# Kernel optimization log

Measured on AMD Instinct MI355X. Metric: run time of the kernel, lower is better.

## Reference

```python
import jax, jax.numpy as jnp
import numpy as np

V, C, H, L, E, D, B, T = 32000, 1024, 16, 3, 8, 1024, 8, 512
FF = 4 * C
EPS = 1e-5


def setup_inputs() -> dict:
    key = jax.random.key(0)
    ks = iter(jax.random.split(key, 32))
    def w(shape, s=0.02):
        return jax.random.normal(next(ks), shape, jnp.float32) * s
    return {
        "idx": jax.random.randint(next(ks), (B, T), 0, V),
        "tok_emb": w((V, C)),
        "ln1_g": jnp.ones((L, C)), "ln1_b": jnp.zeros((L, C)),
        "ln2_g": jnp.ones((L, C)), "ln2_b": jnp.zeros((L, C)),
        "qkv_w": w((L, C, 3 * C)), "proj_w": w((L, C, C)),
        "ff_w1": w((L, C, FF)), "ff_b1": jnp.zeros((L, FF)),
        "ff_w2": w((L, FF, C)), "ff_b2": jnp.zeros((L, C)),
        "router_w": w((C, E)),
        "exp_w1": w((E, C, D)), "exp_b1": jnp.zeros((E, D)),
        "exp_w2": w((E, D, C)), "exp_b2": jnp.zeros((E, C)),
        "lnf_g": jnp.ones((C,)), "lnf_b": jnp.zeros((C,)),
        "head_w": w((C, V)),
    }


def layernorm(x, g, b):
    m = x.mean(-1, keepdims=True)
    v = x.var(-1, keepdims=True)
    return (x - m) * jax.lax.rsqrt(v + EPS) * g + b


def rope_cos_sin(t, d):
    inv = 1.0 / (10000.0 ** (jnp.arange(0, d, 2, dtype=jnp.float32) / d))
    fr = jnp.arange(t, dtype=jnp.float32)[:, None] * inv[None, :]  # [T, d/2]
    emb = jnp.concatenate([fr, fr], -1)  # [T, d]
    return jnp.cos(emb), jnp.sin(emb)


def rot_half(x):
    x1, x2 = jnp.split(x, 2, axis=-1)
    return jnp.concatenate([-x2, x1], -1)


def attn(x, qkv_w, proj_w):
    b, t, c = x.shape
    d = c // H
    qkv = (x @ qkv_w).reshape(b, t, 3, H, d).transpose(2, 0, 3, 1, 4)  # [3,B,H,T,d]
    q, k, v = qkv[0], qkv[1], qkv[2]
    cos, sin = rope_cos_sin(t, d)
    q = q * cos + rot_half(q) * sin
    k = k * cos + rot_half(k) * sin
    s = jnp.einsum('bhqd,bhkd->bhqk', q, k) / np.float32(np.sqrt(d))
    causal = jnp.tril(jnp.ones((t, t), bool))
    s = jnp.where(causal, s, jnp.float32(-1e30))
    a = jax.nn.softmax(s, -1)
    y = jnp.einsum('bhqk,bhkd->bhqd', a, v)
    y = y.transpose(0, 2, 1, 3).reshape(b, t, c)
    return y @ proj_w


def moe(xf, router_w, exp_w1, exp_b1, exp_w2, exp_b2):
    # router softmax -> top-2 -> renormalize -> scatter into dense [N,E] mask
    probs = jax.nn.softmax(xf @ router_w, -1)
    tw, ti = jax.lax.top_k(probs, 2)
    tw = tw / tw.sum(-1, keepdims=True)
    n = xf.shape[0]
    mask = jnp.zeros((n, E), xf.dtype).at[jnp.arange(n)[:, None], ti].set(tw)
    # per-expert dense FFN over all tokens, combined with sparse weights
    h = jax.nn.gelu(jnp.einsum('nc,ecd->end', xf, exp_w1) + exp_b1[:, None, :], approximate=False)
    y = jnp.einsum('end,edc->enc', h, exp_w2) + exp_b2[:, None, :]
    return jnp.einsum('ne,enc->nc', mask, y)


def reference(idx, tok_emb, ln1_g, ln1_b, ln2_g, ln2_b, qkv_w, proj_w,
              ff_w1, ff_b1, ff_w2, ff_b2, router_w, exp_w1, exp_b1,
              exp_w2, exp_b2, lnf_g, lnf_b, head_w):
    x = tok_emb[idx]  # [B,T,C]
    for l in range(L):
        x = x + attn(layernorm(x, ln1_g[l], ln1_b[l]), qkv_w[l], proj_w[l])
        h = layernorm(x, ln2_g[l], ln2_b[l])
        x = x + (jax.nn.gelu(h @ ff_w1[l] + ff_b1[l], approximate=False) @ ff_w2[l] + ff_b2[l])
    b, t, c = x.shape
    x = moe(x.reshape(b * t, c), router_w, exp_w1, exp_b1, exp_w2, exp_b2).reshape(b, t, c)
    x = layernorm(x, lnf_g, lnf_b)
    return x @ head_w  # logits [B,T,V]
```

## Files before the change

kernel.cpp:

```cpp
#include <hip/hip_runtime.h>
#include <math.h>


#define NTOK  4096
#define CDIM  1024
#define HEADS 16
#define DHEAD 64
#define LAYERS 3
#define NEXP  8
#define DEXP  1024
#define TSEQ  512
#define FFDIM 4096
#define VOCAB 32000
#define C3    3072

typedef __attribute__((ext_vector_type(8))) short short8;
typedef __attribute__((ext_vector_type(4))) float f32x4;

__device__ __forceinline__ unsigned short f2bf(float f) {
  unsigned int u = __builtin_bit_cast(unsigned int, f);
  return (unsigned short)((u + 0x7fffu + ((u >> 16) & 1u)) >> 16);
}
__device__ __forceinline__ float bf2f(unsigned short h) {
  return __builtin_bit_cast(float, ((unsigned int)h) << 16);
}

__global__ __launch_bounds__(256) void embed_kernel(const int* __restrict__ idx,
                                                    const float* __restrict__ emb,
                                                    float* __restrict__ x) {
  int i = blockIdx.x * 256 + threadIdx.x;
  int n = i >> 8, c4 = i & 255;
  const float4* src = (const float4*)(emb + (size_t)idx[n] * CDIM);
  ((float4*)(x + (size_t)n * CDIM))[c4] = src[c4];
}

__global__ void rope_table_kernel(float* __restrict__ ct, float* __restrict__ st) {
  int t = blockIdx.x, p = threadIdx.x;
  float inv = powf(10000.0f, -(float)p / 32.0f);
  float ang = (float)t * inv;
  ct[t * 32 + p] = cosf(ang);
  st[t * 32 + p] = sinf(ang);
}

__global__ __launch_bounds__(256) void qkv_prep_kernel(
    const float* __restrict__ qkv, const float* __restrict__ ct,
    const float* __restrict__ st,
    unsigned short* __restrict__ Qh, unsigned short* __restrict__ Qm,
    unsigned short* __restrict__ Ql,
    unsigned short* __restrict__ Kh, unsigned short* __restrict__ Km,
    unsigned short* __restrict__ Kl,
    unsigned short* __restrict__ Vth, unsigned short* __restrict__ Vtm,
    unsigned short* __restrict__ Vtl) {
  __shared__ unsigned short sVh[64 * 64], sVm[64 * 64], sVl[64 * 64];
  const int tid = threadIdx.x;
  const int tt0 = blockIdx.x * 64, h = blockIdx.y, b = blockIdx.z;
  const int bh = b * HEADS + h;
#pragma unroll
  for (int u = 0; u < 8; u++) {
    int pidx = tid + u * 256;
    int tl = pidx >> 5, p = pidx & 31;
    int t = tt0 + tl;
    size_t nb = ((size_t)(b * TSEQ + t)) * C3 + h * DHEAD;
    float c0 = ct[t * 32 + p], s0 = st[t * 32 + p];
    size_t ob = ((size_t)bh * TSEQ + t) * 64;
    float a = qkv[nb + p], bb = qkv[nb + p + 32];
    float lo = a * c0 - bb * s0, hi = bb * c0 + a * s0;
    unsigned short w0, w1;
    float r;
    w0 = f2bf(lo); r = lo - bf2f(w0); w1 = f2bf(r); r -= bf2f(w1);
    Qh[ob + p] = w0; Qm[ob + p] = w1; Ql[ob + p] = f2bf(r);
    w0 = f2bf(hi); r = hi - bf2f(w0); w1 = f2bf(r); r -= bf2f(w1);
    Qh[ob + p + 32] = w0; Qm[ob + p + 32] = w1; Ql[ob + p + 32] = f2bf(r);
    a = qkv[nb + CDIM + p]; bb = qkv[nb + CDIM + p + 32];
    lo = a * c0 - bb * s0; hi = bb * c0 + a * s0;
    w0 = f2bf(lo); r = lo - bf2f(w0); w1 = f2bf(r); r -= bf2f(w1);
    Kh[ob + p] = w0; Km[ob + p] = w1; Kl[ob + p] = f2bf(r);
    w0 = f2bf(hi); r = hi - bf2f(w0); w1 = f2bf(r); r -= bf2f(w1);
    Kh[ob + p + 32] = w0; Km[ob + p + 32] = w1; Kl[ob + p + 32] = f2bf(r);
  }
#pragma unroll
  for (int u = 0; u < 4; u++) {
    int vidx = tid + u * 256;
    int tl = vidx >> 4, d4 = (vidx & 15) * 4;
    int t = tt0 + tl;
    float4 v = *(const float4*)(qkv + ((size_t)(b * TSEQ + t)) * C3 + 2 * CDIM + h * DHEAD + d4);
    float vv[4] = {v.x, v.y, v.z, v.w};
#pragma unroll
    for (int j = 0; j < 4; j++) {
      unsigned short w0 = f2bf(vv[j]);
      float r = vv[j] - bf2f(w0);
      unsigned short w1 = f2bf(r);
      r -= bf2f(w1);
      sVh[(d4 + j) * 64 + tl] = w0;
      sVm[(d4 + j) * 64 + tl] = w1;
      sVl[(d4 + j) * 64 + tl] = f2bf(r);
    }
  }
  __syncthreads();
#pragma unroll
  for (int u = 0; u < 2; u++) {
    int idx = tid + u * 256;
    int d = idx >> 3, seg = (idx & 7) * 8;
    size_t go = ((size_t)bh * 64 + d) * TSEQ + tt0 + seg;
    *(short8*)(Vth + go) = *(const short8*)(sVh + d * 64 + seg);
    *(short8*)(Vtm + go) = *(const short8*)(sVm + d * 64 + seg);
    *(short8*)(Vtl + go) = *(const short8*)(sVl + d * 64 + seg);
  }
}

__global__ __launch_bounds__(256) void flash_attn_kernel(
    const unsigned short* __restrict__ Qh, const unsigned short* __restrict__ Qm,
    const unsigned short* __restrict__ Ql,
    const unsigned short* __restrict__ Kh, const unsigned short* __restrict__ Km,
    const unsigned short* __restrict__ Kl,
    const unsigned short* __restrict__ Vth, const unsigned short* __restrict__ Vtm,
    const unsigned short* __restrict__ Vtl,
    unsigned short* __restrict__ ath, unsigned short* __restrict__ atl) {
  __shared__ __align__(16) unsigned short sK[3][2][64 * 32];
  __shared__ __align__(16) unsigned short sV[3][2][64 * 32];
  __shared__ __align__(16) unsigned short sP[3][2][4][16 * 32];
  const int tid = threadIdx.x;
  const int wv = tid >> 6, ln = tid & 63;
  const int qt = blockIdx.x, h = blockIdx.y, b = blockIdx.z;
  const int bh = b * HEADS + h;
  const int lr = ln & 15, lg = ln >> 4;
  const int q0 = qt * 64 + wv * 16;

  const size_t qoff = ((size_t)bh * TSEQ + q0 + lr) * 64 + 8 * lg;
  short8 qf[3][2];
  qf[0][0] = *(const short8*)(Qh + qoff); qf[0][1] = *(const short8*)(Qh + qoff + 32);
  qf[1][0] = *(const short8*)(Qm + qoff); qf[1][1] = *(const short8*)(Qm + qoff + 32);
  qf[2][0] = *(const short8*)(Ql + qoff); qf[2][1] = *(const short8*)(Ql + qoff + 32);

  f32x4 Y[4];
#pragma unroll
  for (int j = 0; j < 4; j++) Y[j] = (f32x4){0.f, 0.f, 0.f, 0.f};
  float m[4] = {-1e30f, -1e30f, -1e30f, -1e30f};
  float l[4] = {0.f, 0.f, 0.f, 0.f};

  const int r0 = tid >> 3, sg = (tid & 7) * 8;
  const int half = sg >> 5, soff = (sg & 31);

  for (int kt = 0; kt <= qt; kt++) {
    const int kb = kt * 64;
    short8 stg[12];
#pragma unroll
    for (int u = 0; u < 2; u++) {
      int row = r0 + 32 * u;
      size_t gk = ((size_t)bh * TSEQ + kb + row) * 64 + sg;
      size_t gv = ((size_t)bh * 64 + row) * TSEQ + kb + sg;
      stg[u * 6 + 0] = *(const short8*)(Kh + gk);
      stg[u * 6 + 1] = *(const short8*)(Km + gk);
      stg[u * 6 + 2] = *(const short8*)(Kl + gk);
      stg[u * 6 + 3] = *(const short8*)(Vth + gv);
      stg[u * 6 + 4] = *(const short8*)(Vtm + gv);
      stg[u * 6 + 5] = *(const short8*)(Vtl + gv);
    }
    __syncthreads();
#pragma unroll
    for (int u = 0; u < 2; u++) {
      int off = (r0 + 32 * u) * 32 + soff;
      *(short8*)(&sK[0][half][off]) = stg[u * 6 + 0];
      *(short8*)(&sK[1][half][off]) = stg[u * 6 + 1];
      *(short8*)(&sK[2][half][off]) = stg[u * 6 + 2];
      *(short8*)(&sV[0][half][off]) = stg[u * 6 + 3];
      *(short8*)(&sV[1][half][off]) = stg[u * 6 + 4];
      *(short8*)(&sV[2][half][off]) = stg[u * 6 + 5];
    }
    __syncthreads();

    f32x4 s[4];
#pragma unroll
    for (int j = 0; j < 4; j++) s[j] = (f32x4){0.f, 0.f, 0.f, 0.f};
#pragma unroll
    for (int j = 0; j < 4; j++) {
      const int ko = (16 * j + lr) * 32 + 8 * lg;
      short8 k0[3], k1[3];
#pragma unroll
      for (int lv = 0; lv < 3; lv++) {
        k0[lv] = *(const short8*)(&sK[lv][0][ko]);
        k1[lv] = *(const short8*)(&sK[lv][1][ko]);
      }
      s[j] = __builtin_amdgcn_mfma_f32_16x16x32_bf16(qf[0][0], k0[0], s[j], 0, 0, 0);
      s[j] = __builtin_amdgcn_mfma_f32_16x16x32_bf16(qf[0][1], k1[0], s[j], 0, 0, 0);
      s[j] = __builtin_amdgcn_mfma_f32_16x16x32_bf16(qf[0][0], k0[1], s[j], 0, 0, 0);
      s[j] = __builtin_amdgcn_mfma_f32_16x16x32_bf16(qf[0][1], k1[1], s[j], 0, 0, 0);
      s[j] = __builtin_amdgcn_mfma_f32_16x16x32_bf16(qf[1][0], k0[0], s[j], 0, 0, 0);
      s[j] = __builtin_amdgcn_mfma_f32_16x16x32_bf16(qf[1][1], k1[0], s[j], 0, 0, 0);
      s[j] = __builtin_amdgcn_mfma_f32_16x16x32_bf16(qf[0][0], k0[2], s[j], 0, 0, 0);
      s[j] = __builtin_amdgcn_mfma_f32_16x16x32_bf16(qf[0][1], k1[2], s[j], 0, 0, 0);
      s[j] = __builtin_amdgcn_mfma_f32_16x16x32_bf16(qf[1][0], k0[1], s[j], 0, 0, 0);
      s[j] = __builtin_amdgcn_mfma_f32_16x16x32_bf16(qf[1][1], k1[1], s[j], 0, 0, 0);
      s[j] = __builtin_amdgcn_mfma_f32_16x16x32_bf16(qf[2][0], k0[0], s[j], 0, 0, 0);
      s[j] = __builtin_amdgcn_mfma_f32_16x16x32_bf16(qf[2][1], k1[0], s[j], 0, 0, 0);
    }

    const bool diag = (kt == qt);
#pragma unroll
    for (int rr = 0; rr < 4; rr++) {
      const int q = q0 + 4 * lg + rr;
      float mx = -1e30f;
#pragma unroll
      for (int j = 0; j < 4; j++) {
        float v = s[j][rr] * 0.125f;
        if (diag && (kb + 16 * j + lr > q)) v = -1e30f;
        s[j][rr] = v;
        mx = fmaxf(mx, v);
      }
      mx = fmaxf(mx, __shfl_xor(mx, 1));
      mx = fmaxf(mx, __shfl_xor(mx, 2));
      mx = fmaxf(mx, __shfl_xor(mx, 4));
      mx = fmaxf(mx, __shfl_xor(mx, 8));
      float mn = fmaxf(m[rr], mx);
      float al = expf(m[rr] - mn);
      m[rr] = mn;
      l[rr] *= al;
#pragma unroll
      for (int j = 0; j < 4; j++) Y[j][rr] *= al;
      float ps = 0.f;
#pragma unroll
      for (int j = 0; j < 4; j++) {
        float p = expf(s[j][rr] - mn);
        s[j][rr] = p;
        ps += p;
      }
      l[rr] += ps;
    }

#pragma unroll
    for (int j = 0; j < 4; j++) {
      const int jh = j >> 1;
      const int col = 16 * (j & 1) + lr;
#pragma unroll
      for (int rr = 0; rr < 4; rr++) {
        float p = s[j][rr];
        unsigned short w0 = f2bf(p);
        float r = p - bf2f(w0);
        unsigned short w1 = f2bf(r);
        r -= bf2f(w1);
        const int o = (4 * lg + rr) * 32 + col;
        sP[0][jh][wv][o] = w0;
        sP[1][jh][wv][o] = w1;
        sP[2][jh][wv][o] = f2bf(r);
      }
    }
    __syncthreads();
    const int po = lr * 32 + 8 * lg;
    short8 pf[3][2];
#pragma unroll
    for (int lv = 0; lv < 3; lv++) {
      pf[lv][0] = *(const short8*)(&sP[lv][0][wv][po]);
      pf[lv][1] = *(const short8*)(&sP[lv][1][wv][po]);
    }
#pragma unroll
    for (int jd = 0; jd < 4; jd++) {
      const int vo = (16 * jd + lr) * 32 + 8 * lg;
      short8 v0[3], v1[3];
#pragma unroll
      for (int lv = 0; lv < 3; lv++) {
        v0[lv] = *(const short8*)(&sV[lv][0][vo]);
        v1[lv] = *(const short8*)(&sV[lv][1][vo]);
      }
      Y[jd] = __builtin_amdgcn_mfma_f32_16x16x32_bf16(pf[0][0], v0[0], Y[jd], 0, 0, 0);
      Y[jd] = __builtin_amdgcn_mfma_f32_16x16x32_bf16(pf[0][1], v1[0], Y[jd], 0, 0, 0);
      Y[jd] = __builtin_amdgcn_mfma_f32_16x16x32_bf16(pf[0][0], v0[1], Y[jd], 0, 0, 0);
      Y[jd] = __builtin_amdgcn_mfma_f32_16x16x32_bf16(pf[0][1], v1[1], Y[jd], 0, 0, 0);
      Y[jd] = __builtin_amdgcn_mfma_f32_16x16x32_bf16(pf[1][0], v0[0], Y[jd], 0, 0, 0);
      Y[jd] = __builtin_amdgcn_mfma_f32_16x16x32_bf16(pf[1][1], v1[0], Y[jd], 0, 0, 0);
      Y[jd] = __builtin_amdgcn_mfma_f32_16x16x32_bf16(pf[0][0], v0[2], Y[jd], 0, 0, 0);
      Y[jd] = __builtin_amdgcn_mfma_f32_16x16x32_bf16(pf[0][1], v1[2], Y[jd], 0, 0, 0);
      Y[jd] = __builtin_amdgcn_mfma_f32_16x16x32_bf16(pf[1][0], v0[1], Y[jd], 0, 0, 0);
      Y[jd] = __builtin_amdgcn_mfma_f32_16x16x32_bf16(pf[1][1], v1[1], Y[jd], 0, 0, 0);
      Y[jd] = __builtin_amdgcn_mfma_f32_16x16x32_bf16(pf[2][0], v0[0], Y[jd], 0, 0, 0);
      Y[jd] = __builtin_amdgcn_mfma_f32_16x16x32_bf16(pf[2][1], v1[0], Y[jd], 0, 0, 0);
    }
  }

#pragma unroll
  for (int rr = 0; rr < 4; rr++) {
    float t = l[rr];
    t += __shfl_xor(t, 1); t += __shfl_xor(t, 2);
    t += __shfl_xor(t, 4); t += __shfl_xor(t, 8);
    l[rr] = 1.0f / t;
  }
#pragma unroll
  for (int jd = 0; jd < 4; jd++) {
    const int d = 16 * jd + lr;
#pragma unroll
    for (int rr = 0; rr < 4; rr++) {
      const int q = q0 + 4 * lg + rr;
      float v = Y[jd][rr] * l[rr];
      unsigned short w0 = f2bf(v);
      const size_t ci = ((size_t)(b * TSEQ + q)) * CDIM + h * DHEAD + d;
      ath[ci] = w0;
      atl[ci] = f2bf(v - bf2f(w0));
    }
  }
}

__global__ __launch_bounds__(256) void ln_split_kernel(const float* __restrict__ x,
                                                       unsigned short* __restrict__ yh,
                                                       unsigned short* __restrict__ yl,
                                                       const float* __restrict__ g,
                                                       const float* __restrict__ b) {
  int n = blockIdx.x, tid = threadIdx.x;
  const float4* xr = (const float4*)(x + (size_t)n * CDIM);
  float4 v = xr[tid];
  float s = v.x + v.y + v.z + v.w;
  float ss = v.x * v.x + v.y * v.y + v.z * v.z + v.w * v.w;
  __shared__ float rs[256], rss[256];
  rs[tid] = s; rss[tid] = ss;
  __syncthreads();
  for (int o = 128; o > 0; o >>= 1) {
    if (tid < o) { rs[tid] += rs[tid + o]; rss[tid] += rss[tid + o]; }
    __syncthreads();
  }
  float m = rs[0] * (1.0f / CDIM);
  float var = rss[0] * (1.0f / CDIM) - m * m;
  float r = rsqrtf(var + 1e-5f);
  float4 gv = ((const float4*)g)[tid];
  float4 bv = ((const float4*)b)[tid];
  float o0 = (v.x - m) * r * gv.x + bv.x;
  float o1 = (v.y - m) * r * gv.y + bv.y;
  float o2 = (v.z - m) * r * gv.z + bv.z;
  float o3 = (v.w - m) * r * gv.w + bv.w;
  ushort4 hh, ll;
  hh.x = f2bf(o0); ll.x = f2bf(o0 - bf2f(hh.x));
  hh.y = f2bf(o1); ll.y = f2bf(o1 - bf2f(hh.y));
  hh.z = f2bf(o2); ll.z = f2bf(o2 - bf2f(hh.z));
  hh.w = f2bf(o3); ll.w = f2bf(o3 - bf2f(hh.w));
  ((ushort4*)(yh + (size_t)n * CDIM))[tid] = hh;
  ((ushort4*)(yl + (size_t)n * CDIM))[tid] = ll;
}

__global__ __launch_bounds__(256) void cvt_bf16_kernel(const float* __restrict__ x,
                                                       unsigned short* __restrict__ y) {
  int i = blockIdx.x * 256 + threadIdx.x;
  float4 v = ((const float4*)x)[i];
  ushort4 o;
  o.x = f2bf(v.x); o.y = f2bf(v.y); o.z = f2bf(v.z); o.w = f2bf(v.w);
  ((ushort4*)y)[i] = o;
}

__global__ __launch_bounds__(256) void ln_bf16_kernel(const float* __restrict__ x,
                                                      unsigned short* __restrict__ y,
                                                      const float* __restrict__ g,
                                                      const float* __restrict__ b) {
  int n = blockIdx.x, tid = threadIdx.x;
  const float4* xr = (const float4*)(x + (size_t)n * CDIM);
  float4 v = xr[tid];
  float s = v.x + v.y + v.z + v.w;
  float ss = v.x * v.x + v.y * v.y + v.z * v.z + v.w * v.w;
  __shared__ float rs[256], rss[256];
  rs[tid] = s; rss[tid] = ss;
  __syncthreads();
  for (int o = 128; o > 0; o >>= 1) {
    if (tid < o) { rs[tid] += rs[tid + o]; rss[tid] += rss[tid + o]; }
    __syncthreads();
  }
  float m = rs[0] * (1.0f / CDIM);
  float var = rss[0] * (1.0f / CDIM) - m * m;
  float r = rsqrtf(var + 1e-5f);
  float4 gv = ((const float4*)g)[tid];
  float4 bv = ((const float4*)b)[tid];
  ushort4 o4;
  o4.x = f2bf((v.x - m) * r * gv.x + bv.x);
  o4.y = f2bf((v.y - m) * r * gv.y + bv.y);
  o4.z = f2bf((v.z - m) * r * gv.z + bv.z);
  o4.w = f2bf((v.w - m) * r * gv.w + bv.w);
  ((ushort4*)(y + (size_t)n * CDIM))[tid] = o4;
}

__global__ __launch_bounds__(256) void wconv_t_kernel(const float* __restrict__ W,
                                                      unsigned short* __restrict__ Wt,
                                                      int K, int N) {
  __shared__ float t[32][33];
  int n0 = blockIdx.x * 32, k0 = blockIdx.y * 32;
  int tx = threadIdx.x & 31, ty = threadIdx.x >> 5;
#pragma unroll
  for (int i = 0; i < 4; i++)
    t[ty + 8 * i][tx] = W[(size_t)(k0 + ty + 8 * i) * N + n0 + tx];
  __syncthreads();
#pragma unroll
  for (int i = 0; i < 4; i++)
    Wt[(size_t)(n0 + ty + 8 * i) * K + k0 + tx] = f2bf(t[tx][ty + 8 * i]);
}

__global__ __launch_bounds__(256) void wconv_split_kernel(const float* __restrict__ W,
                                                          unsigned short* __restrict__ Wh,
                                                          unsigned short* __restrict__ Wl,
                                                          int K, int N) {
  __shared__ float t[32][33];
  int n0 = blockIdx.x * 32, k0 = blockIdx.y * 32;
  int tx = threadIdx.x & 31, ty = threadIdx.x >> 5;
#pragma unroll
  for (int i = 0; i < 4; i++)
    t[ty + 8 * i][tx] = W[(size_t)(k0 + ty + 8 * i) * N + n0 + tx];
  __syncthreads();
#pragma unroll
  for (int i = 0; i < 4; i++) {
    float w = t[tx][ty + 8 * i];
    unsigned short h = f2bf(w);
    size_t o = (size_t)(n0 + ty + 8 * i) * K + k0 + tx;
    Wh[o] = h;
    Wl[o] = f2bf(w - bf2f(h));
  }
}

__device__ __forceinline__ void xcd_swz(int& bx, int& by) {
  int bid = blockIdx.y * gridDim.x + blockIdx.x;
  int cpx = (gridDim.x * gridDim.y) >> 3;
  bid = (bid & 7) * cpx + (bid >> 3);
  bx = bid % gridDim.x;
  by = bid / gridDim.x;
}

template <int MODE>
__global__ __launch_bounds__(256) void gemm_split(const unsigned short* __restrict__ Ah,
                                                  const unsigned short* __restrict__ Al,
                                                  const unsigned short* __restrict__ Bth,
                                                  const unsigned short* __restrict__ Btl,
                                                  float* __restrict__ C,
                                                  unsigned short* __restrict__ Ch,
                                                  unsigned short* __restrict__ Cl,
                                                  const float* __restrict__ bias,
                                                  int M, int Nn, int K) {
  __shared__ __align__(16) unsigned short AsH[128 * 32];
  __shared__ __align__(16) unsigned short AsL[128 * 32];
  __shared__ __align__(16) unsigned short BsH[128 * 32];
  __shared__ __align__(16) unsigned short BsL[128 * 32];
  const int tid = threadIdx.x;
  const int wv = tid >> 6, ln = tid & 63;
  int sbx, sby;
  xcd_swz(sbx, sby);
  const int bm = sby * 128, bn = sbx * 128;

  const size_t aoff0 = (size_t)(bm + 32 * wv + (ln >> 2)) * K + (size_t)((ln & 3) * 8);
  const size_t aoff1 = aoff0 + (size_t)16 * K;
  const size_t boff0 = (size_t)(bn + 32 * wv + (ln >> 2)) * K + (size_t)((ln & 3) * 8);
  const size_t boff1 = boff0 + (size_t)16 * K;
  const int lofs = 1024 * wv + ln * 8;

  const int wm = wv >> 1, wn = wv & 1;
  const int lr = ln & 15, lg = ln >> 4;

  f32x4 acc[4][4];
#pragma unroll
  for (int i = 0; i < 4; i++)
#pragma unroll
    for (int j = 0; j < 4; j++) acc[i][j] = (f32x4){0.f, 0.f, 0.f, 0.f};

  for (int k0 = 0; k0 < K; k0 += 32) {
    short8 rah0 = *(const short8*)(Ah + aoff0 + k0);
    short8 rah1 = *(const short8*)(Ah + aoff1 + k0);
    short8 ral0 = *(const short8*)(Al + aoff0 + k0);
    short8 ral1 = *(const short8*)(Al + aoff1 + k0);
    short8 rbh0 = *(const short8*)(Bth + boff0 + k0);
    short8 rbh1 = *(const short8*)(Bth + boff1 + k0);
    short8 rbl0 = *(const short8*)(Btl + boff0 + k0);
    short8 rbl1 = *(const short8*)(Btl + boff1 + k0);
    __syncthreads();
    *(short8*)(AsH + lofs)       = rah0;
    *(short8*)(AsH + lofs + 512) = rah1;
    *(short8*)(AsL + lofs)       = ral0;
    *(short8*)(AsL + lofs + 512) = ral1;
    *(short8*)(BsH + lofs)       = rbh0;
    *(short8*)(BsH + lofs + 512) = rbh1;
    *(short8*)(BsL + lofs)       = rbl0;
    *(short8*)(BsL + lofs + 512) = rbl1;
    __syncthreads();

    short8 afh[4], afl[4], bwh[4], bwl[4];
#pragma unroll
    for (int i = 0; i < 4; i++) {
      const int ao = (64 * wm + 16 * i + lr) * 32 + 8 * lg;
      afh[i] = *(const short8*)(AsH + ao);
      afl[i] = *(const short8*)(AsL + ao);
    }
#pragma unroll
    for (int j = 0; j < 4; j++) {
      const int bo = (64 * wn + 16 * j + lr) * 32 + 8 * lg;
      bwh[j] = *(const short8*)(BsH + bo);
      bwl[j] = *(const short8*)(BsL + bo);
    }
#pragma unroll
    for (int i = 0; i < 4; i++)
#pragma unroll
      for (int j = 0; j < 4; j++) {
        acc[i][j] = __builtin_amdgcn_mfma_f32_16x16x32_bf16(afh[i], bwh[j], acc[i][j], 0, 0, 0);
        acc[i][j] = __builtin_amdgcn_mfma_f32_16x16x32_bf16(afl[i], bwh[j], acc[i][j], 0, 0, 0);
        acc[i][j] = __builtin_amdgcn_mfma_f32_16x16x32_bf16(afh[i], bwl[j], acc[i][j], 0, 0, 0);
      }
  }

#pragma unroll
  for (int j = 0; j < 4; j++) {
    const int n = bn + 64 * wn + 16 * j + lr;
    const float bb = (MODE == 1 || MODE == 3) ? bias[n] : 0.0f;
#pragma unroll
    for (int i = 0; i < 4; i++) {
#pragma unroll
      for (int rr = 0; rr < 4; rr++) {
        const int m = bm + 64 * wm + 16 * i + 4 * lg + rr;
        float v = acc[i][j][rr];
        const size_t ci = (size_t)m * Nn + n;
        if constexpr (MODE == 0) {
          C[ci] = v;
        } else if constexpr (MODE == 1) {
          v += bb;
          v = 0.5f * v * (1.0f + erff(v * 0.70710678118654752f));
          unsigned short h = f2bf(v);
          Ch[ci] = h;
          Cl[ci] = f2bf(v - bf2f(h));
        } else if constexpr (MODE == 2) {
          C[ci] += v;
        } else {
          C[ci] += v + bb;
        }
      }
    }
  }
}

template <int MODE>
__global__ __launch_bounds__(256) void gemm_bf16(const unsigned short* __restrict__ A,
                                                 const unsigned short* __restrict__ Bt,
                                                 float* __restrict__ C,
                                                 unsigned short* __restrict__ Cu,
                                                 const float* __restrict__ bias,
                                                 const float* __restrict__ rowscale,
                                                 int M, int Nn, int K) {
  __shared__ __align__(16) unsigned short As[128 * 32];
  __shared__ __align__(16) unsigned short Bs[128 * 32];
  const int tid = threadIdx.x;
  const int wv = tid >> 6, ln = tid & 63;
  int sbx, sby;
  xcd_swz(sbx, sby);
  const int bm = sby * 128, bn = sbx * 128;

  const size_t aoff0 = (size_t)(bm + 32 * wv + (ln >> 2)) * K + (size_t)((ln & 3) * 8);
  const size_t aoff1 = aoff0 + (size_t)16 * K;
  const size_t boff0 = (size_t)(bn + 32 * wv + (ln >> 2)) * K + (size_t)((ln & 3) * 8);
  const size_t boff1 = boff0 + (size_t)16 * K;
  const int lofs = 1024 * wv + ln * 8;

  const int wm = wv >> 1, wn = wv & 1;
  const int lr = ln & 15, lg = ln >> 4;

  f32x4 acc[4][4];
#pragma unroll
  for (int i = 0; i < 4; i++)
#pragma unroll
    for (int j = 0; j < 4; j++) acc[i][j] = (f32x4){0.f, 0.f, 0.f, 0.f};

  for (int k0 = 0; k0 < K; k0 += 32) {
    short8 ra0 = *(const short8*)(A + aoff0 + k0);
    short8 ra1 = *(const short8*)(A + aoff1 + k0);
    short8 rb0 = *(const short8*)(Bt + boff0 + k0);
    short8 rb1 = *(const short8*)(Bt + boff1 + k0);
    __syncthreads();
    *(short8*)(As + lofs)       = ra0;
    *(short8*)(As + lofs + 512) = ra1;
    *(short8*)(Bs + lofs)       = rb0;
    *(short8*)(Bs + lofs + 512) = rb1;
    __syncthreads();

    short8 af[4], bw[4];
#pragma unroll
    for (int i = 0; i < 4; i++)
      af[i] = *(const short8*)(As + ((64 * wm + 16 * i + lr) * 32 + 8 * lg));
#pragma unroll
    for (int j = 0; j < 4; j++)
      bw[j] = *(const short8*)(Bs + ((64 * wn + 16 * j + lr) * 32 + 8 * lg));
#pragma unroll
    for (int i = 0; i < 4; i++)
#pragma unroll
      for (int j = 0; j < 4; j++)
        acc[i][j] = __builtin_amdgcn_mfma_f32_16x16x32_bf16(af[i], bw[j], acc[i][j], 0, 0, 0);
  }

#pragma unroll
  for (int j = 0; j < 4; j++) {
    const int n = bn + 64 * wn + 16 * j + lr;
    const float bb = (MODE != 0) ? bias[n] : 0.0f;
#pragma unroll
    for (int i = 0; i < 4; i++) {
#pragma unroll
      for (int r = 0; r < 4; r++) {
        const int m = bm + 64 * wm + 16 * i + 4 * lg + r;
        float v = acc[i][j][r];
        const size_t ci = (size_t)m * Nn + n;
        if constexpr (MODE == 0) {
          C[ci] = v;
        } else if constexpr (MODE == 1) {
          v += bb;
          v = 0.5f * v * (1.0f + erff(v * 0.70710678118654752f));
          Cu[ci] = f2bf(v);
        } else {
          C[ci] += rowscale[m] * (v + bb);
        }
      }
    }
  }
}

__global__ __launch_bounds__(64) void router_kernel(const float* __restrict__ x,
                                                    const float* __restrict__ rw,
                                                    float* __restrict__ maskT) {
  int n = blockIdx.x, lane = threadIdx.x;
  const float* xr = x + (size_t)n * CDIM;
  float acc[NEXP] = {};
  for (int i = 0; i < CDIM / 64; i++) {
    int c = lane + 64 * i;
    float xv = xr[c];
    const float* r = rw + (size_t)c * NEXP;
#pragma unroll
    for (int e = 0; e < NEXP; e++) acc[e] += xv * r[e];
  }
  for (int m = 32; m >= 1; m >>= 1)
#pragma unroll
    for (int e = 0; e < NEXP; e++) acc[e] += __shfl_xor(acc[e], m);
  if (lane == 0) {
    float mx = acc[0];
#pragma unroll
    for (int e = 1; e < NEXP; e++) mx = fmaxf(mx, acc[e]);
    float p[NEXP];
#pragma unroll
    for (int e = 0; e < NEXP; e++) p[e] = expf(acc[e] - mx);
    int i1 = 0;
#pragma unroll
    for (int e = 1; e < NEXP; e++) if (p[e] > p[i1]) i1 = e;
    int i2 = (i1 == 0) ? 1 : 0;
#pragma unroll
    for (int e = 0; e < NEXP; e++) if (e != i1 && p[e] > p[i2]) i2 = e;
    float denom = p[i1] + p[i2];
    float w1 = p[i1] / denom, w2 = p[i2] / denom;
#pragma unroll
    for (int e = 0; e < NEXP; e++) maskT[(size_t)e * NTOK + n] = 0.0f;
    maskT[(size_t)i1 * NTOK + n] = w1;
    maskT[(size_t)i2 * NTOK + n] = w2;
  }
}

extern "C" void kernel_launch(void* const* d_in, const int* in_sizes, int n_in,
                              void* d_out, int out_size, void* d_ws, size_t ws_size,
                              hipStream_t stream) {
  const int*   idx      = (const int*)d_in[0];
  const float* tok_emb  = (const float*)d_in[1];
  const float* ln1_g    = (const float*)d_in[2];
  const float* ln1_b    = (const float*)d_in[3];
  const float* ln2_g    = (const float*)d_in[4];
  const float* ln2_b    = (const float*)d_in[5];
  const float* qkv_w    = (const float*)d_in[6];
  const float* proj_w   = (const float*)d_in[7];
  const float* ff_w1    = (const float*)d_in[8];
  const float* ff_b1    = (const float*)d_in[9];
  const float* ff_w2    = (const float*)d_in[10];
  const float* ff_b2    = (const float*)d_in[11];
  const float* router_w = (const float*)d_in[12];
  const float* exp_w1   = (const float*)d_in[13];
  const float* exp_b1   = (const float*)d_in[14];
  const float* exp_w2   = (const float*)d_in[15];
  const float* exp_b2   = (const float*)d_in[16];
  const float* lnf_g    = (const float*)d_in[17];
  const float* lnf_b    = (const float*)d_in[18];
  const float* head_w   = (const float*)d_in[19];
  float* out = (float*)d_out;

  const size_t NC = (size_t)NTOK * CDIM;
  char* w = (char*)d_ws;
  float* x  = (float*)w;                 w += NC * 4;
  unsigned short* S1 = (unsigned short*)w; w += NC * 4;
  float* Q  = (float*)w;                 w += (size_t)NTOK * C3 * 4;
  float* C3r = (float*)w;                w += NC * 4;
  unsigned short* WS = (unsigned short*)w; w += NC * 4;
  unsigned short* EX = (unsigned short*)w; w += NC * 6;
  float* maskT = (float*)w;              w += (size_t)NEXP * NTOK * 4;
  float* ct = (float*)w;                 w += (size_t)TSEQ * 32 * 4;
  float* st = (float*)w;                 w += (size_t)TSEQ * 32 * 4;

  unsigned short* xh = S1;
  unsigned short* xl = S1 + NC;
  unsigned short* Wh = WS;
  unsigned short* Wl = WS + NC;
  float* qkvf = Q;
  unsigned short* Qh_s = S1;
  unsigned short* Qm_s = S1 + NC;
  unsigned short* Ql_s = EX;
  unsigned short* Kh_s = (unsigned short*)C3r;
  unsigned short* Km_s = (unsigned short*)C3r + NC;
  unsigned short* Kl_s = EX + NC;
  unsigned short* Vth_s = WS;
  unsigned short* Vtm_s = WS + NC;
  unsigned short* Vtl_s = EX + 2 * NC;
  unsigned short* ath = (unsigned short*)Q;
  unsigned short* atl = (unsigned short*)Q + NC;
  unsigned short* hh = (unsigned short*)Q;
  unsigned short* hl = (unsigned short*)Q + (size_t)NTOK * FFDIM;
  unsigned short* x_bf    = S1;
  unsigned short* hmoe_bf = S1 + NC;
  float* moe_out  = x;
  unsigned short* wt_s = WS;
  unsigned short* xn_bf   = S1;
  unsigned short* wt_head = (unsigned short*)Q;

  embed_kernel<<<NTOK, 256, 0, stream>>>(idx, tok_emb, x);
  rope_table_kernel<<<TSEQ, 32, 0, stream>>>(ct, st);

  for (int l = 0; l < LAYERS; l++) {
    ln_split_kernel<<<NTOK, 256, 0, stream>>>(x, xh, xl, ln1_g + l * CDIM, ln1_b + l * CDIM);
    wconv_split_kernel<<<dim3(C3 / 32, CDIM / 32), 256, 0, stream>>>(
        qkv_w + (size_t)l * CDIM * C3, Wh, Wl, CDIM, C3);
    gemm_split<0><<<dim3(C3 / 128, NTOK / 128), 256, 0, stream>>>(
        xh, xl, Wh, Wl, qkvf, nullptr, nullptr, nullptr, NTOK, C3, CDIM);
    qkv_prep_kernel<<<dim3(TSEQ / 64, HEADS, 8), 256, 0, stream>>>(
        qkvf, ct, st, Qh_s, Qm_s, Ql_s, Kh_s, Km_s, Kl_s, Vth_s, Vtm_s, Vtl_s);
    flash_attn_kernel<<<dim3(TSEQ / 64, HEADS, 8), 256, 0, stream>>>(
        Qh_s, Qm_s, Ql_s, Kh_s, Km_s, Kl_s, Vth_s, Vtm_s, Vtl_s, ath, atl);
    wconv_split_kernel<<<dim3(CDIM / 32, CDIM / 32), 256, 0, stream>>>(
        proj_w + (size_t)l * CDIM * CDIM, Wh, Wl, CDIM, CDIM);
    gemm_split<2><<<dim3(CDIM / 128, NTOK / 128), 256, 0, stream>>>(
        ath, atl, Wh, Wl, x, nullptr, nullptr, nullptr, NTOK, CDIM, CDIM);
    ln_split_kernel<<<NTOK, 256, 0, stream>>>(x, xh, xl, ln2_g + l * CDIM, ln2_b + l * CDIM);
    wconv_split_kernel<<<dim3(FFDIM / 32, CDIM / 32), 256, 0, stream>>>(
        ff_w1 + (size_t)l * CDIM * FFDIM, Wh, Wl, CDIM, FFDIM);
    gemm_split<1><<<dim3(FFDIM / 128, NTOK / 128), 256, 0, stream>>>(
        xh, xl, Wh, Wl, nullptr, hh, hl, ff_b1 + (size_t)l * FFDIM, NTOK, FFDIM, CDIM);
    wconv_split_kernel<<<dim3(CDIM / 32, FFDIM / 32), 256, 0, stream>>>(
        ff_w2 + (size_t)l * FFDIM * CDIM, Wh, Wl, FFDIM, CDIM);
    gemm_split<3><<<dim3(CDIM / 128, NTOK / 128), 256, 0, stream>>>(
        hh, hl, Wh, Wl, x, nullptr, nullptr, ff_b2 + (size_t)l * CDIM, NTOK, CDIM, FFDIM);
  }

  router_kernel<<<NTOK, 64, 0, stream>>>(x, router_w, maskT);
  cvt_bf16_kernel<<<(NC / 4) / 256, 256, 0, stream>>>(x, x_bf);
  hipMemsetAsync(moe_out, 0, NC * sizeof(float), stream);
  for (int e = 0; e < NEXP; e++) {
    wconv_t_kernel<<<dim3(DEXP / 32, CDIM / 32), 256, 0, stream>>>(
        exp_w1 + (size_t)e * CDIM * DEXP, wt_s, CDIM, DEXP);
    gemm_bf16<1><<<dim3(DEXP / 128, NTOK / 128), 256, 0, stream>>>(
        x_bf, wt_s, nullptr, hmoe_bf, exp_b1 + (size_t)e * DEXP, nullptr, NTOK, DEXP, CDIM);
    wconv_t_kernel<<<dim3(CDIM / 32, DEXP / 32), 256, 0, stream>>>(
        exp_w2 + (size_t)e * DEXP * CDIM, wt_s, DEXP, CDIM);
    gemm_bf16<2><<<dim3(CDIM / 128, NTOK / 128), 256, 0, stream>>>(
        hmoe_bf, wt_s, moe_out, nullptr, exp_b2 + (size_t)e * CDIM,
        maskT + (size_t)e * NTOK, NTOK, CDIM, DEXP);
  }

  ln_bf16_kernel<<<NTOK, 256, 0, stream>>>(moe_out, xn_bf, lnf_g, lnf_b);
  wconv_t_kernel<<<dim3(VOCAB / 32, CDIM / 32), 256, 0, stream>>>(head_w, wt_head, CDIM, VOCAB);
  gemm_bf16<0><<<dim3(VOCAB / 128, NTOK / 128), 256, 0, stream>>>(
      xn_bf, wt_head, out, nullptr, nullptr, nullptr, NTOK, VOCAB, CDIM);
}
```

Measured before the change: 2.865 ms.

## Route MoE tokens via per-expert gather lists instead of dense all-token expert GEMMs

```diff
diff --git a/kernel.cpp b/kernel.cpp
--- a/kernel.cpp
+++ b/kernel.cpp
@@ -522,13 +522,9 @@
   }
 }
 
-template <int MODE>
 __global__ __launch_bounds__(256) void gemm_bf16(const unsigned short* __restrict__ A,
                                                  const unsigned short* __restrict__ Bt,
                                                  float* __restrict__ C,
-                                                 unsigned short* __restrict__ Cu,
-                                                 const float* __restrict__ bias,
-                                                 const float* __restrict__ rowscale,
                                                  int M, int Nn, int K) {
   __shared__ __align__(16) unsigned short As[128 * 32];
   __shared__ __align__(16) unsigned short Bs[128 * 32];
@@ -582,31 +578,173 @@
 #pragma unroll
   for (int j = 0; j < 4; j++) {
     const int n = bn + 64 * wn + 16 * j + lr;
-    const float bb = (MODE != 0) ? bias[n] : 0.0f;
 #pragma unroll
     for (int i = 0; i < 4; i++) {
 #pragma unroll
       for (int r = 0; r < 4; r++) {
         const int m = bm + 64 * wm + 16 * i + 4 * lg + r;
-        float v = acc[i][j][r];
-        const size_t ci = (size_t)m * Nn + n;
-        if constexpr (MODE == 0) {
-          C[ci] = v;
-        } else if constexpr (MODE == 1) {
-          v += bb;
-          v = 0.5f * v * (1.0f + erff(v * 0.70710678118654752f));
-          Cu[ci] = f2bf(v);
-        } else {
-          C[ci] += rowscale[m] * (v + bb);
+        C[(size_t)m * Nn + n] = acc[i][j][r];
+      }
+    }
+  }
+}
+
+__global__ __launch_bounds__(256) void gemm_moe1(const unsigned short* __restrict__ A,
+                                                 const unsigned short* __restrict__ Bt,
+                                                 unsigned short* __restrict__ Cu,
+                                                 const float* __restrict__ bias,
+                                                 const int* __restrict__ cnt,
+                                                 const int* __restrict__ lst,
+                                                 int Nn, int K) {
+  const int ce = *cnt;
+  const int bm = blockIdx.y * 128, bn = blockIdx.x * 128;
+  if (bm >= ce) return;
+  __shared__ __align__(16) unsigned short As[128 * 32];
+  __shared__ __align__(16) unsigned short Bs[128 * 32];
+  const int tid = threadIdx.x;
+  const int wv = tid >> 6, ln = tid & 63;
+
+  const int ra = bm + 32 * wv + (ln >> 2);
+  const int t0 = lst[(ra      < ce) ? ra      : 0];
+  const int t1 = lst[(ra + 16 < ce) ? ra + 16 : 0];
+  const size_t aoff0 = (size_t)t0 * K + (size_t)((ln & 3) * 8);
+  const size_t aoff1 = (size_t)t1 * K + (size_t)((ln & 3) * 8);
+  const size_t boff0 = (size_t)(bn + 32 * wv + (ln >> 2)) * K + (size_t)((ln & 3) * 8);
+  const size_t boff1 = boff0 + (size_t)16 * K;
+  const int lofs = 1024 * wv + ln * 8;
+
+  const int wm = wv >> 1, wn = wv & 1;
+  const int lr = ln & 15, lg = ln >> 4;
+
+  f32x4 acc[4][4];
+#pragma unroll
+  for (int i = 0; i < 4; i++)
+#pragma unroll
+    for (int j = 0; j < 4; j++) acc[i][j] = (f32x4){0.f, 0.f, 0.f, 0.f};
+
+  for (int k0 = 0; k0 < K; k0 += 32) {
+    short8 ra0 = *(const short8*)(A + aoff0 + k0);
+    short8 ra1 = *(const short8*)(A + aoff1 + k0);
+    short8 rb0 = *(const short8*)(Bt + boff0 + k0);
+    short8 rb1 = *(const short8*)(Bt + boff1 + k0);
+    __syncthreads();
+    *(short8*)(As + lofs)       = ra0;
+    *(short8*)(As + lofs + 512) = ra1;
+    *(short8*)(Bs + lofs)       = rb0;
+    *(short8*)(Bs + lofs + 512) = rb1;
+    __syncthreads();
+
+    short8 af[4], bw[4];
+#pragma unroll
+    for (int i = 0; i < 4; i++)
+      af[i] = *(const short8*)(As + ((64 * wm + 16 * i + lr) * 32 + 8 * lg));
+#pragma unroll
+    for (int j = 0; j < 4; j++)
+      bw[j] = *(const short8*)(Bs + ((64 * wn + 16 * j + lr) * 32 + 8 * lg));
+#pragma unroll
+    for (int i = 0; i < 4; i++)
+#pragma unroll
+      for (int j = 0; j < 4; j++)
+        acc[i][j] = __builtin_amdgcn_mfma_f32_16x16x32_bf16(af[i], bw[j], acc[i][j], 0, 0, 0);
+  }
+
+#pragma unroll
+  for (int j = 0; j < 4; j++) {
+    const int n = bn + 64 * wn + 16 * j + lr;
+    const float bb = bias[n];
+#pragma unroll
+    for (int i = 0; i < 4; i++) {
+#pragma unroll
+      for (int r = 0; r < 4; r++) {
+        const int m = bm + 64 * wm + 16 * i + 4 * lg + r;
+        float v = acc[i][j][r] + bb;
+        v = 0.5f * v * (1.0f + erff(v * 0.70710678118654752f));
+        Cu[(size_t)m * Nn + n] = f2bf(v);
+      }
+    }
+  }
+}
+
+__global__ __launch_bounds__(256) void gemm_moe2(const unsigned short* __restrict__ A,
+                                                 const unsigned short* __restrict__ Bt,
+                                                 float* __restrict__ C,
+                                                 const float* __restrict__ bias,
+                                                 const int* __restrict__ cnt,
+                                                 const int* __restrict__ lst,
+                                                 const float* __restrict__ wts,
+                                                 int Nn, int K) {
+  const int ce = *cnt;
+  const int bm = blockIdx.y * 128, bn = blockIdx.x * 128;
+  if (bm >= ce) return;
+  __shared__ __align__(16) unsigned short As[128 * 32];
+  __shared__ __align__(16) unsigned short Bs[128 * 32];
+  const int tid = threadIdx.x;
+  const int wv = tid >> 6, ln = tid & 63;
+
+  const size_t aoff0 = (size_t)(bm + 32 * wv + (ln >> 2)) * K + (size_t)((ln & 3) * 8);
+  const size_t aoff1 = aoff0 + (size_t)16 * K;
+  const size_t boff0 = (size_t)(bn + 32 * wv + (ln >> 2)) * K + (size_t)((ln & 3) * 8);
+  const size_t boff1 = boff0 + (size_t)16 * K;
+  const int lofs = 1024 * wv + ln * 8;
+
+  const int wm = wv >> 1, wn = wv & 1;
+  const int lr = ln & 15, lg = ln >> 4;
+
+  f32x4 acc[4][4];
+#pragma unroll
+  for (int i = 0; i < 4; i++)
+#pragma unroll
+    for (int j = 0; j < 4; j++) acc[i][j] = (f32x4){0.f, 0.f, 0.f, 0.f};
+
+  for (int k0 = 0; k0 < K; k0 += 32) {
+    short8 ra0 = *(const short8*)(A + aoff0 + k0);
+    short8 ra1 = *(const short8*)(A + aoff1 + k0);
+    short8 rb0 = *(const short8*)(Bt + boff0 + k0);
+    short8 rb1 = *(const short8*)(Bt + boff1 + k0);
+    __syncthreads();
+    *(short8*)(As + lofs)       = ra0;
+    *(short8*)(As + lofs + 512) = ra1;
+    *(short8*)(Bs + lofs)       = rb0;
+    *(short8*)(Bs + lofs + 512) = rb1;
+    __syncthreads();
+
+    short8 af[4], bw[4];
+#pragma unroll
+    for (int i = 0; i < 4; i++)
+      af[i] = *(const short8*)(As + ((64 * wm + 16 * i + lr) * 32 + 8 * lg));
+#pragma unroll
+    for (int j = 0; j < 4; j++)
+      bw[j] = *(const short8*)(Bs + ((64 * wn + 16 * j + lr) * 32 + 8 * lg));
+#pragma unroll
+    for (int i = 0; i < 4; i++)
+#pragma unroll
+      for (int j = 0; j < 4; j++)
+        acc[i][j] = __builtin_amdgcn_mfma_f32_16x16x32_bf16(af[i], bw[j], acc[i][j], 0, 0, 0);
+  }
+
+#pragma unroll
+  for (int j = 0; j < 4; j++) {
+    const int n = bn + 64 * wn + 16 * j + lr;
+    const float bb = bias[n];
+#pragma unroll
+    for (int i = 0; i < 4; i++) {
+#pragma unroll
+      for (int r = 0; r < 4; r++) {
+        const int m = bm + 64 * wm + 16 * i + 4 * lg + r;
+        if (m < ce) {
+          const int tok = lst[m];
+          C[(size_t)tok * Nn + n] += wts[m] * (acc[i][j][r] + bb);
         }
       }
     }
   }
 }
 
-__global__ __launch_bounds__(64) void router_kernel(const float* __restrict__ x,
-                                                    const float* __restrict__ rw,
-                                                    float* __restrict__ maskT) {
+__global__ __launch_bounds__(64) void router2_kernel(const float* __restrict__ x,
+                                                     const float* __restrict__ rw,
+                                                     int* __restrict__ cnt,
+                                                     int* __restrict__ lst,
+                                                     float* __restrict__ wts) {
   int n = blockIdx.x, lane = threadIdx.x;
   const float* xr = x + (size_t)n * CDIM;
   float acc[NEXP] = {};
@@ -634,11 +772,12 @@
 #pragma unroll
     for (int e = 0; e < NEXP; e++) if (e != i1 && p[e] > p[i2]) i2 = e;
     float denom = p[i1] + p[i2];
-    float w1 = p[i1] / denom, w2 = p[i2] / denom;
-#pragma unroll
-    for (int e = 0; e < NEXP; e++) maskT[(size_t)e * NTOK + n] = 0.0f;
-    maskT[(size_t)i1 * NTOK + n] = w1;
-    maskT[(size_t)i2 * NTOK + n] = w2;
+    int p1 = atomicAdd(&cnt[i1], 1);
+    lst[i1 * NTOK + p1] = n;
+    wts[i1 * NTOK + p1] = p[i1] / denom;
+    int p2 = atomicAdd(&cnt[i2], 1);
+    lst[i2 * NTOK + p2] = n;
+    wts[i2 * NTOK + p2] = p[i2] / denom;
   }
 }
 
@@ -675,9 +814,11 @@
   float* C3r = (float*)w;                w += NC * 4;
   unsigned short* WS = (unsigned short*)w; w += NC * 4;
   unsigned short* EX = (unsigned short*)w; w += NC * 6;
-  float* maskT = (float*)w;              w += (size_t)NEXP * NTOK * 4;
   float* ct = (float*)w;                 w += (size_t)TSEQ * 32 * 4;
   float* st = (float*)w;                 w += (size_t)TSEQ * 32 * 4;
+  int*   moe_cnt = (int*)w;              w += NEXP * 4;
+  int*   moe_lst = (int*)w;              w += (size_t)NEXP * NTOK * 4;
+  float* moe_wts = (float*)w;            w += (size_t)NEXP * NTOK * 4;
 
   unsigned short* xh = S1;
   unsigned short* xl = S1 + NC;
@@ -732,23 +873,26 @@
         hh, hl, Wh, Wl, x, nullptr, nullptr, ff_b2 + (size_t)l * CDIM, NTOK, CDIM, FFDIM);
   }
 
-  router_kernel<<<NTOK, 64, 0, stream>>>(x, router_w, maskT);
+  hipMemsetAsync(moe_cnt, 0, NEXP * sizeof(int), stream);
+  router2_kernel<<<NTOK, 64, 0, stream>>>(x, router_w, moe_cnt, moe_lst, moe_wts);
   cvt_bf16_kernel<<<(NC / 4) / 256, 256, 0, stream>>>(x, x_bf);
   hipMemsetAsync(moe_out, 0, NC * sizeof(float), stream);
   for (int e = 0; e < NEXP; e++) {
     wconv_t_kernel<<<dim3(DEXP / 32, CDIM / 32), 256, 0, stream>>>(
         exp_w1 + (size_t)e * CDIM * DEXP, wt_s, CDIM, DEXP);
-    gemm_bf16<1><<<dim3(DEXP / 128, NTOK / 128), 256, 0, stream>>>(
-        x_bf, wt_s, nullptr, hmoe_bf, exp_b1 + (size_t)e * DEXP, nullptr, NTOK, DEXP, CDIM);
+    gemm_moe1<<<dim3(DEXP / 128, NTOK / 128), 256, 0, stream>>>(
+        x_bf, wt_s, hmoe_bf, exp_b1 + (size_t)e * DEXP,
+        moe_cnt + e, moe_lst + (size_t)e * NTOK, DEXP, CDIM);
     wconv_t_kernel<<<dim3(CDIM / 32, DEXP / 32), 256, 0, stream>>>(
         exp_w2 + (size_t)e * DEXP * CDIM, wt_s, DEXP, CDIM);
-    gemm_bf16<2><<<dim3(CDIM / 128, NTOK / 128), 256, 0, stream>>>(
-        hmoe_bf, wt_s, moe_out, nullptr, exp_b2 + (size_t)e * CDIM,
-        maskT + (size_t)e * NTOK, NTOK, CDIM, DEXP);
+    gemm_moe2<<<dim3(CDIM / 128, NTOK / 128), 256, 0, stream>>>(
+        hmoe_bf, wt_s, moe_out, exp_b2 + (size_t)e * CDIM,
+        moe_cnt + e, moe_lst + (size_t)e * NTOK, moe_wts + (size_t)e * NTOK,
+        CDIM, DEXP);
   }
 
   ln_bf16_kernel<<<NTOK, 256, 0, stream>>>(moe_out, xn_bf, lnf_g, lnf_b);
   wconv_t_kernel<<<dim3(VOCAB / 32, CDIM / 32), 256, 0, stream>>>(head_w, wt_head, CDIM, VOCAB);
-  gemm_bf16<0><<<dim3(VOCAB / 128, NTOK / 128), 256, 0, stream>>>(
-      xn_bf, wt_head, out, nullptr, nullptr, nullptr, NTOK, VOCAB, CDIM);
-}
+  gemm_bf16<<<dim3(VOCAB / 128, NTOK / 128), 256, 0, stream>>>(
+      xn_bf, wt_head, out, NTOK, VOCAB, CDIM);
+}
```

Result: slower. 3.038 ms (+6.0%).
